# Kernel tuning notes

Measured on AMD Instinct MI355X. Metric: run time of the kernel, lower is better.

Reference implementation:

```python
import jax, jax.numpy as jnp
import numpy as np
from jax import lax

# ---- config (FalconH1Mixer, FalconH1-1.5B-like) ----
BATCH = 2
SEQ = 2048
HID = 2048
EXPAND = 2
INTER = EXPAND * HID          # 4096 (mamba_d_ssm=None)
HEADS = 64
PDIM = INTER // HEADS         # 64 head_dim
NSTATE = 128                  # mamba_d_state
G = 1                         # mamba_n_groups
HPG = HEADS // G
KCONV = 4                     # mamba_d_conv
GTS = G * NSTATE
CONV_DIM = INTER + 2 * GTS    # 4352
PROJ_DIM = 2 * INTER + 2 * GTS + HEADS  # 8512 (z | xBC | dt)
EPS = 1e-5
MUP = (0.25, 0.5, 0.5, 0.5, 1.0)  # ssm_multipliers for z, x, B, C, dt


def _mup_vector():
    # per-region muP multipliers over the zxbcdt projection axis
    return jnp.concatenate([
        jnp.full((INTER,), MUP[0], jnp.float32),
        jnp.full((INTER,), MUP[1], jnp.float32),
        jnp.full((GTS,), MUP[2], jnp.float32),
        jnp.full((GTS,), MUP[3], jnp.float32),
        jnp.full((HEADS,), MUP[4], jnp.float32),
    ])


def setup_inputs() -> dict:
    key = jax.random.key(0)
    ks = jax.random.split(key, 8)
    hidden_states = jax.random.normal(ks[0], (BATCH, SEQ, HID), jnp.float32)
    in_proj_w = jax.random.normal(ks[1], (HID, PROJ_DIM), jnp.float32) * 0.02
    conv_w = jax.random.normal(ks[2], (CONV_DIM, KCONV), jnp.float32) * 0.2
    conv_b = jnp.zeros((CONV_DIM,), jnp.float32)
    A_log = jnp.log(jnp.arange(1, HEADS + 1, dtype=jnp.float32))
    D = jnp.ones((HEADS,), jnp.float32)
    dt_bias = jax.random.uniform(ks[3], (HEADS,), jnp.float32)
    norm_w = jnp.ones((INTER,), jnp.float32)
    out_proj_w = jax.random.normal(ks[4], (INTER, HID), jnp.float32) * 0.02
    return dict(hidden_states=hidden_states, in_proj_w=in_proj_w, conv_w=conv_w,
                conv_b=conv_b, A_log=A_log, D=D, dt_bias=dt_bias,
                norm_w=norm_w, out_proj_w=out_proj_w)


def _forward(hidden_states, in_proj_w, conv_w, conv_b, A_log, D, dt_bias, norm_w, out_proj_w):
    b, l, _ = hidden_states.shape
    # zxbcdt projection with muP scaling
    proj = (hidden_states @ in_proj_w) * _mup_vector()  # (b, l, PROJ_DIM)
    z = proj[..., :INTER]
    xBC = proj[..., INTER:INTER + CONV_DIM]
    dt = proj[..., INTER + CONV_DIM:]                    # (b, l, HEADS)
    # depthwise causal conv1d + SiLU
    xBC_cl = jnp.swapaxes(xBC, 1, 2)                     # (b, c, l)
    conv = lax.conv_general_dilated(xBC_cl, conv_w[:, None, :],
                                    window_strides=(1,), padding=((KCONV - 1, 0),),
                                    feature_group_count=CONV_DIM)
    xBC = jax.nn.silu(jnp.swapaxes(conv + conv_b[None, :, None], 1, 2))  # (b, l, c)
    x = xBC[..., :INTER].reshape(b, l, G, HPG, PDIM)
    Bm = xBC[..., INTER:INTER + GTS].reshape(b, l, G, NSTATE)
    Cm = xBC[..., INTER + GTS:].reshape(b, l, G, NSTATE)
    # dt / A discretization
    dt = jax.nn.softplus(dt + dt_bias)                   # (b, l, HEADS)
    A = -jnp.exp(A_log)                                  # (HEADS,)
    dA = jnp.exp(dt * A).reshape(b, l, G, HPG)           # (b, l, g, c)
    dtx = dt.reshape(b, l, G, HPG)[..., None] * x        # (b, l, g, c, p)

    def step(state, inp):
        dA_t, dtx_t, B_t, C_t = inp                      # (b,g,c) (b,g,c,p) (b,g,n) (b,g,n)
        state = state * dA_t[..., None, None] + jnp.einsum('bgcp,bgn->bgcpn', dtx_t, B_t)
        y_t = jnp.einsum('bgn,bgcpn->bgcp', C_t, state)
        return state, y_t

    inputs = (jnp.moveaxis(dA, 1, 0), jnp.moveaxis(dtx, 1, 0),
              jnp.moveaxis(Bm, 1, 0), jnp.moveaxis(Cm, 1, 0))
    state0 = jnp.zeros((b, G, HPG, PDIM, NSTATE), hidden_states.dtype)
    _, ys = lax.scan(step, state0, inputs)               # (l, b, g, c, p)
    y = jnp.moveaxis(ys, 0, 1) + D.reshape(1, 1, G, HPG, 1) * x
    y = y.reshape(b, l, INTER)
    # grouped RMSNorm, then SiLU gate (norm_before_gate=True)
    yg = y.reshape(b, l, G, INTER // G)
    var = jnp.mean(jnp.square(yg), axis=-1, keepdims=True)
    yn = (yg * lax.rsqrt(var + EPS)).reshape(b, l, INTER) * norm_w
    out = yn * jax.nn.silu(z)
    return out @ out_proj_w                              # (b, l, HID)


def reference(hidden_states, in_proj_w, conv_w, conv_b, A_log, D, dt_bias, norm_w, out_proj_w):
    return _forward(hidden_states, in_proj_w, conv_w, conv_b, A_log, D, dt_bias, norm_w, out_proj_w)
```

## Files before the change

### kernel.cpp

```cpp
#include <hip/hip_runtime.h>
#include <stdint.h>

typedef unsigned short u16;
typedef unsigned int   u32;
typedef __attribute__((ext_vector_type(8))) short bf16x8;
typedef __attribute__((ext_vector_type(4))) float f32x4;
typedef __attribute__((ext_vector_type(4))) u32   u32x4;

static __device__ __forceinline__ float bf2f(u16 v){
  u32 u = ((u32)v) << 16;
  return __builtin_bit_cast(float, u);
}
static __device__ __forceinline__ u16 f2bf(float f){
  u32 u = __builtin_bit_cast(u32, f);
  return (u16)((u + 0x7fffu + ((u >> 16) & 1u)) >> 16);
}

#define MFMA16(a,b,c) __builtin_amdgcn_mfma_f32_16x16x32_bf16((a),(b),(c),0,0,0)

typedef const __attribute__((address_space(1))) char glb_c;
typedef __attribute__((address_space(3))) char lds_c;
static __device__ __forceinline__ void gload_lds16(const void* g, void* l){
  __builtin_amdgcn_global_load_lds((glb_c*)g, (lds_c*)l, 16, 0, 0);
}

#define SEQN   2048
#define PROJD  8512
#define CONVD  4352
#define INTERD 4096
#define NST    128
#define QC     64
#define NCHUNK 32

__global__ __launch_bounds__(256) void detect_kernel(
    const void* __restrict__ hidden, u32* __restrict__ flag)
{
  __shared__ int cnt;
  if (threadIdx.x == 0) cnt = 0;
  __syncthreads();
  if (threadIdx.x < 128){
    u16 v = ((const u16*)hidden)[threadIdx.x * 2];
    int e = (v >> 7) & 0xFF;
    int plaus = (v == 0) || (e >= 0x70 && e <= 0x8F);
    atomicAdd(&cnt, plaus);
  }
  __syncthreads();
  if (threadIdx.x == 0) *flag = (cnt < 64) ? 1u : 0u;
}

__global__ __launch_bounds__(256) void cvt_kernel(
    const void* __restrict__ src, u16* __restrict__ dst, int n,
    const u32* __restrict__ flag)
{
  bool isf32 = (*flag != 0);
  int stride = gridDim.x * 256;
  for (int i = blockIdx.x*256 + threadIdx.x; i < n; i += stride){
    if (isf32) dst[i] = f2bf(((const float*)src)[i]);
    else       dst[i] = ((const u16*)src)[i];
  }
}

__global__ __launch_bounds__(256) void cvt_transpose_kernel(
    const void* __restrict__ src, u16* __restrict__ dst,
    int K, int N, int Npad, const u32* __restrict__ flag)
{
  bool isf32 = (*flag != 0);
  __shared__ u16 tile[64][72];
  int n0 = blockIdx.x * 64, k0 = blockIdx.y * 64;
  int tid = threadIdx.x;
  int tr = tid >> 6;
  int tc = tid & 63;
  #pragma unroll
  for (int i = 0; i < 16; i++){
    int k = i*4 + tr;
    int gk = k0 + k, gn = n0 + tc;
    float v = 0.f;
    if (gk < K && gn < N)
      v = isf32 ? ((const float*)src)[(size_t)gk*N + gn]
                : bf2f(((const u16*)src)[(size_t)gk*N + gn]);
    tile[k][tc] = f2bf(v);
  }
  __syncthreads();
  #pragma unroll
  for (int i = 0; i < 16; i++){
    int n = i*4 + tr;
    int gn = n0 + n;
    if (gn < Npad && (k0 + tc) < K)
      dst[(size_t)gn*K + k0 + tc] = tile[tc][n];
  }
}

__global__ __launch_bounds__(256) void cvt_small_kernel(
    const void* cw, const void* cb, const void* al, const void* dv,
    const void* db, const void* nw, u16* __restrict__ base,
    const u32* __restrict__ flag)
{
  bool isf32 = (*flag != 0);
  int idx = blockIdx.x*256 + threadIdx.x;
  if (idx >= 26048) return;
  const void* src; int off;
  if      (idx < 17408){ src = cw; off = idx;          }
  else if (idx < 21760){ src = cb; off = idx - 17408;  }
  else if (idx < 21824){ src = al; off = idx - 21760;  }
  else if (idx < 21888){ src = dv; off = idx - 21824;  }
  else if (idx < 21952){ src = db; off = idx - 21888;  }
  else                 { src = nw; off = idx - 21952;  }
  u16 v = isf32 ? f2bf(((const float*)src)[off]) : ((const u16*)src)[off];
  base[idx] = v;
}

__global__ __launch_bounds__(512, 2) void gemm_kernel(
    const u16* __restrict__ A, const u16* __restrict__ Bt,
    u16* __restrict__ C0, u16* __restrict__ C1, u16* __restrict__ C2,
    float* __restrict__ CF,
    int M, int N, int K, int mode)
{
  __shared__ u16 smem[65536];

  const int nbx = gridDim.x;
  const int nwg = nbx * gridDim.y;
  const int bid = blockIdx.y * nbx + blockIdx.x;
  const int swz = (bid & 7) * (nwg >> 3) + (bid >> 3);
  const int m0 = (swz / nbx) * 256, n0 = (swz % nbx) * 256;

  const int tid = threadIdx.x;
  const int wave = tid >> 6, lane = tid & 63;
  const int l15 = lane & 15, quad = lane >> 4;
  const int wm = wave >> 2, wn = wave & 3;

  const size_t Kb = (size_t)K * 2;
  const int srow = tid >> 3;
  const int schk = (tid & 7) ^ (srow & 7);
  const char* Abp = (const char*)A  + (size_t)(m0 + srow) * Kb + schk * 16;
  const char* Bbp = (const char*)Bt + (size_t)(n0 + srow) * Kb + schk * 16;
  char* ldsb = (char*)smem + wave * 1024;

  const int aoff0 = ((quad    ) ^ (l15 & 7)) << 4;
  const int aoff1 = ((quad + 4) ^ (l15 & 7)) << 4;
  const char* ardb[2][2];
  const char* brdb[2][2];
  #pragma unroll
  for (int c = 0; c < 2; c++){
    ardb[c][0] = (const char*)smem + c*65536 + (wm*128 + l15)*128 + aoff0;
    ardb[c][1] = (const char*)smem + c*65536 + (wm*128 + l15)*128 + aoff1;
    brdb[c][0] = (const char*)smem + c*65536 + 32768 + (wn*64 + l15)*128 + aoff0;
    brdb[c][1] = (const char*)smem + c*65536 + 32768 + (wn*64 + l15)*128 + aoff1;
  }

  f32x4 acc[8][4];
  #pragma unroll
  for (int i = 0; i < 8; i++)
    #pragma unroll
    for (int j = 0; j < 4; j++) acc[i][j] = (f32x4){0.f,0.f,0.f,0.f};

  bf16x8 af[4];
  bf16x8 bfr[8];

#define STG(ptr, par, isB, h, kt) do{                                    \
    const char* _s = (ptr) + (size_t)((h)*128)*Kb + (size_t)(kt)*128;    \
    char* _d = ldsb + (par)*65536 + ((isB)?32768:0) + (h)*16384;         \
    gload_lds16(_s, _d);                                                 \
    gload_lds16(_s + 64*Kb, _d + 8192);                                  \
  }while(0)

  STG(Bbp,0,1,0,0); STG(Bbp,0,1,1,0);
  STG(Abp,0,0,0,0); STG(Abp,0,0,1,0);
  STG(Bbp,1,1,0,1); STG(Bbp,1,1,1,1);
  asm volatile("s_waitcnt vmcnt(4)" ::: "memory");
  __builtin_amdgcn_s_barrier();

  const int NT = K >> 6;
  for (int I = 0; I < (NT >> 1); ++I){
    const int T1 = 2*I+1, T2 = 2*I+2, T3 = 2*I+3;
    const bool pf = (T2 < NT);
    #pragma unroll
    for (int p = 0; p < 8; ++p){
      const int q = p & 3, c = p >> 2;
      #pragma unroll
      for (int k = 0; k < 2; k++){
        af[0+k] = *(const bf16x8*)(ardb[c][k] + (2*q+0)*2048);
        af[2+k] = *(const bf16x8*)(ardb[c][k] + (2*q+1)*2048);
      }
      if (q == 0){
        #pragma unroll
        for (int nf = 0; nf < 4; nf++)
          #pragma unroll
          for (int k = 0; k < 2; k++)
            bfr[nf*2+k] = *(const bf16x8*)(brdb[c][k] + nf*2048);
      }
      if      (p == 0) STG(Abp,1,0,0,T1);
      else if (p == 1) STG(Abp,1,0,1,T1);
      else if (p == 2){ if (pf) STG(Bbp,0,1,0,T2); }
      else if (p == 3){
        if (pf){ STG(Bbp,0,1,1,T2);
                 asm volatile("s_waitcnt vmcnt(4)" ::: "memory"); }
        else     asm volatile("s_waitcnt vmcnt(0)" ::: "memory");
      }
      else if (p == 4){ if (pf) STG(Abp,0,0,0,T2); }
      else if (p == 5){ if (pf) STG(Abp,0,0,1,T2); }
      else if (p == 6){ if (pf) STG(Bbp,1,1,0,T3); }
      else            { if (pf){ STG(Bbp,1,1,1,T3);
                 asm volatile("s_waitcnt vmcnt(4)" ::: "memory"); } }
      asm volatile("" ::: "memory");
      __builtin_amdgcn_s_barrier();
      asm volatile("s_waitcnt lgkmcnt(0)" ::: "memory");
      __builtin_amdgcn_s_setprio(1);
      #pragma unroll
      for (int mf2 = 0; mf2 < 2; ++mf2)
        #pragma unroll
        for (int nf = 0; nf < 4; ++nf)
          #pragma unroll
          for (int k = 0; k < 2; k++)
            acc[2*q+mf2][nf] =
                MFMA16(af[mf2*2+k], bfr[nf*2+k], acc[2*q+mf2][nf]);
      __builtin_amdgcn_s_setprio(0);
      asm volatile("" ::: "memory");
      __builtin_amdgcn_s_barrier();
    }
  }
#undef STG

  #pragma unroll
  for (int nf = 0; nf < 4; nf++){
    int col = n0 + wn*64 + nf*16 + l15;
    #pragma unroll
    for (int mf = 0; mf < 8; mf++){
      #pragma unroll
      for (int r = 0; r < 4; r++){
        int row = m0 + wm*128 + mf*16 + quad*4 + r;
        float fv = acc[mf][nf][r];
        if (mode == 2){
          if (col < N) CF[(size_t)row*N + col] = fv;
        } else if (mode == 0){
          if (col < N) C0[(size_t)row*N + col] = f2bf(fv);
        } else {
          u16 v = f2bf(fv);
          if      (col < 4096) C0[(size_t)row*4096 + col] = v;
          else if (col < 8448) C1[(size_t)row*CONVD + (col - 4096)] = v;
          else if (col < 8512) C2[(size_t)row*64 + (col - 8448)] = v;
        }
      }
    }
  }
}

__global__ __launch_bounds__(256) void conv_silu_kernel(
    const u16* __restrict__ xbcr, const u16* __restrict__ conv_w,
    const u16* __restrict__ conv_b, u16* __restrict__ xbc)
{
  int c  = blockIdx.x * 256 + threadIdx.x;
  int rl = blockIdx.y;
  int b = rl >> 11, l = rl & 2047;
  float w[4];
  #pragma unroll
  for (int k=0;k<4;k++) w[k] = 0.5f * bf2f(conv_w[c*4 + k]);
  float acc = bf2f(conv_b[c]);
  #pragma unroll
  for (int k=0;k<4;k++){
    int s = l + k - 3;
    if (s >= 0) acc += bf2f(xbcr[(size_t)(b*2048 + s)*CONVD + c]) * w[k];
  }
  float sig = 1.f / (1.f + __expf(-acc));
  xbc[(size_t)rl*CONVD + c] = f2bf(acc * sig);
}

__global__ __launch_bounds__(256) void dt_kernel(
    const u16* __restrict__ dtraw, const u16* __restrict__ dt_bias,
    const u16* __restrict__ A_log, float* __restrict__ dt_soft,
    float* __restrict__ ldA)
{
  int idx = blockIdx.x * 256 + threadIdx.x;
  int h = idx & 63;
  float x = bf2f(dtraw[idx]) + bf2f(dt_bias[h]);
  float sp = (x > 20.f) ? x : log1pf(expf(x));
  float A = -expf(bf2f(A_log[h]));
  dt_soft[idx] = sp;
  ldA[idx] = sp * A;
}

__global__ __launch_bounds__(256) void chunk_decay_kernel(
    const float* __restrict__ ldA, float* __restrict__ cdexp)
{
  int idx = blockIdx.x * 256 + threadIdx.x;
  int q = idx & 31, bh = idx >> 5;
  int b = bh >> 6, h = bh & 63;
  float s = 0.f;
  int t0 = q * QC;
  for (int t = 0; t < QC; t++) s += ldA[(size_t)(b*2048 + t0 + t)*64 + h];
  cdexp[idx] = expf(s);
}

#define SBS  136
#define SUTS 80
#define SMS  80
__global__ __launch_bounds__(256) void ssd_intra_kernel(
    const u16* __restrict__ xbc, const float* __restrict__ dt_soft,
    const float* __restrict__ ldA, u16* __restrict__ S,
    u16* __restrict__ y)
{
  int q = blockIdx.x, h = blockIdx.y, b = blockIdx.z;
  int bh = b*64 + h;
  int t0 = q * QC;
  int tid = threadIdx.x, wave = tid >> 6, lane = tid & 63;
  int l15 = lane & 15, quad = lane >> 4;

  __shared__ u16 sB [64*SBS];
  __shared__ u16 sCM[64*SBS];
  __shared__ u16 sBt[128*64];
  __shared__ u16 sUt[64*SUTS];
  __shared__ float sLa[64];
  __shared__ float sW[64];

  if (tid < 64){
    float v = ldA[(size_t)(b*2048 + t0 + tid)*64 + h];
    #pragma unroll
    for (int off = 1; off < 64; off <<= 1){
      float o = __shfl_up(v, off, 64);
      if (lane >= off) v += o;
    }
    sLa[tid] = v;
  }
  __syncthreads();
  float laE = sLa[63];
  if (tid < 64) sW[tid] = __expf(laE - sLa[tid]);
  __syncthreads();

  #pragma unroll
  for (int i = 0; i < 4; i++){
    int ch = i*256 + tid;
    int s = ch >> 4, nc = (ch & 15) * 8;
    const u16* src = xbc + (size_t)(b*2048 + t0 + s)*CONVD;
    u32x4 vb = *(const u32x4*)(src + 4096 + nc);
    u32x4 vc = *(const u32x4*)(src + 4224 + nc);
    *(u32x4*)(sB  + s*SBS + nc) = vb;
    *(u32x4*)(sCM + s*SBS + nc) = vc;
    float wdec = sW[s];
    const u16* pb = (const u16*)&vb;
    #pragma unroll
    for (int e = 0; e < 8; e++)
      sBt[(nc + e)*64 + s] = f2bf(bf2f(pb[e]) * wdec);
  }
  #pragma unroll
  for (int i = 0; i < 2; i++){
    int ch = i*256 + tid;
    int s = ch >> 3, pc = (ch & 7) * 8;
    const u16* src = xbc + (size_t)(b*2048 + t0 + s)*CONVD + h*64 + pc;
    u32x4 vx = *(const u32x4*)src;
    float dt = dt_soft[(size_t)(b*2048 + t0 + s)*64 + h];
    const u16* px = (const u16*)&vx;
    #pragma unroll
    for (int e = 0; e < 8; e++)
      sUt[(pc + e)*SUTS + s] = f2bf(bf2f(px[e]) * dt);
  }
  __syncthreads();

  int tr = (wave & 1)*32, sc = (wave >> 1)*32;
  f32x4 aM[2][2];
  #pragma unroll
  for (int i=0;i<2;i++)
    #pragma unroll
    for (int j=0;j<2;j++) aM[i][j] = (f32x4){0.f,0.f,0.f,0.f};
  #pragma unroll
  for (int kk = 0; kk < 128; kk += 32){
    bf16x8 a0 = *(const bf16x8*)(sCM + (tr      + l15)*SBS + kk + quad*8);
    bf16x8 a1 = *(const bf16x8*)(sCM + (tr + 16 + l15)*SBS + kk + quad*8);
    bf16x8 b0 = *(const bf16x8*)(sB  + (sc      + l15)*SBS + kk + quad*8);
    bf16x8 b1 = *(const bf16x8*)(sB  + (sc + 16 + l15)*SBS + kk + quad*8);
    aM[0][0] = MFMA16(a0, b0, aM[0][0]);
    aM[0][1] = MFMA16(a0, b1, aM[0][1]);
    aM[1][0] = MFMA16(a1, b0, aM[1][0]);
    aM[1][1] = MFMA16(a1, b1, aM[1][1]);
  }
  __syncthreads();
  u16* sM = sCM;
  #pragma unroll
  for (int i = 0; i < 2; i++){
    #pragma unroll
    for (int j = 0; j < 2; j++){
      int scol = sc + j*16 + l15;
      #pragma unroll
      for (int r = 0; r < 4; r++){
        int trow = tr + i*16 + quad*4 + r;
        float v = 0.f;
        if (scol <= trow) v = aM[i][j][r] * __expf(sLa[trow] - sLa[scol]);
        sM[trow*SMS + scol] = f2bf(v);
      }
    }
  }
  __syncthreads();

  f32x4 aY[2][2];
  #pragma unroll
  for (int i=0;i<2;i++)
    #pragma unroll
    for (int j=0;j<2;j++) aY[i][j] = (f32x4){0.f,0.f,0.f,0.f};
  #pragma unroll
  for (int kk = 0; kk < 64; kk += 32){
    bf16x8 a0 = *(const bf16x8*)(sM  + (tr      + l15)*SMS  + kk + quad*8);
    bf16x8 a1 = *(const bf16x8*)(sM  + (tr + 16 + l15)*SMS  + kk + quad*8);
    bf16x8 b0 = *(const bf16x8*)(sUt + (sc      + l15)*SUTS + kk + quad*8);
    bf16x8 b1 = *(const bf16x8*)(sUt + (sc + 16 + l15)*SUTS + kk + quad*8);
    aY[0][0] = MFMA16(a0, b0, aY[0][0]);
    aY[0][1] = MFMA16(a0, b1, aY[0][1]);
    aY[1][0] = MFMA16(a1, b0, aY[1][0]);
    aY[1][1] = MFMA16(a1, b1, aY[1][1]);
  }
  #pragma unroll
  for (int i = 0; i < 2; i++){
    #pragma unroll
    for (int j = 0; j < 2; j++){
      int p = sc + j*16 + l15;
      #pragma unroll
      for (int r = 0; r < 4; r++){
        int t = tr + i*16 + quad*4 + r;
        y[(size_t)(b*2048 + t0 + t)*INTERD + h*64 + p] = f2bf(aY[i][j][r]);
      }
    }
  }

  int pr = (wave & 1)*32, nw = (wave >> 1)*64;
  f32x4 aS[2][4];
  #pragma unroll
  for (int i=0;i<2;i++)
    #pragma unroll
    for (int j=0;j<4;j++) aS[i][j] = (f32x4){0.f,0.f,0.f,0.f};
  #pragma unroll
  for (int kk = 0; kk < 64; kk += 32){
    bf16x8 a0 = *(const bf16x8*)(sUt + (pr      + l15)*SUTS + kk + quad*8);
    bf16x8 a1 = *(const bf16x8*)(sUt + (pr + 16 + l15)*SUTS + kk + quad*8);
    #pragma unroll
    for (int j = 0; j < 4; j++){
      bf16x8 bb = *(const bf16x8*)(sBt + (nw + j*16 + l15)*64 + kk + quad*8);
      aS[0][j] = MFMA16(a0, bb, aS[0][j]);
      aS[1][j] = MFMA16(a1, bb, aS[1][j]);
    }
  }
  u16* Sl = S + ((size_t)bh*NCHUNK + q)*8192;
  #pragma unroll
  for (int i = 0; i < 2; i++){
    #pragma unroll
    for (int j = 0; j < 4; j++){
      int n = nw + j*16 + l15;
      #pragma unroll
      for (int r = 0; r < 4; r++){
        int p = pr + i*16 + quad*4 + r;
        Sl[p*NST + n] = f2bf(aS[i][j][r]);
      }
    }
  }
}

__global__ __launch_bounds__(256) void ssd_carry_kernel(
    u16* __restrict__ S, const float* __restrict__ cdexp)
{
  int idx = blockIdx.x * 256 + threadIdx.x;
  int e = idx & 8191, bh = idx >> 13;
  float E = 0.f;
  for (int q = 0; q < NCHUNK; q++){
    size_t off = ((size_t)bh*NCHUNK + q)*8192 + e;
    float v = bf2f(S[off]);
    S[off] = f2bf(E);
    E = cdexp[bh*NCHUNK + q] * E + v;
  }
}

__global__ __launch_bounds__(256) void ssd_inter_kernel(
    const u16* __restrict__ xbc, const float* __restrict__ ldA,
    const u16* __restrict__ S, const u16* __restrict__ Dvec,
    u16* __restrict__ y)
{
  int q = blockIdx.x, h = blockIdx.y, b = blockIdx.z;
  int bh = b*64 + h;
  int t0 = q * QC;
  int tid = threadIdx.x, wave = tid >> 6, lane = tid & 63;
  int l15 = lane & 15, quad = lane >> 4;

  __shared__ u16 sC[64*SBS];
  __shared__ u16 sS[64*SBS];
  __shared__ float sLa[64];

  if (tid < 64){
    float v = ldA[(size_t)(b*2048 + t0 + tid)*64 + h];
    #pragma unroll
    for (int off = 1; off < 64; off <<= 1){
      float o = __shfl_up(v, off, 64);
      if (lane >= off) v += o;
    }
    sLa[tid] = v;
  }
  const u16* Sc = S + ((size_t)bh*NCHUNK + q)*8192;
  #pragma unroll
  for (int i = 0; i < 4; i++){
    int ch = i*256 + tid;
    int s = ch >> 4, nc = (ch & 15) * 8;
    *(u32x4*)(sC + s*SBS + nc) =
        *(const u32x4*)(xbc + (size_t)(b*2048 + t0 + s)*CONVD + 4224 + nc);
    *(u32x4*)(sS + s*SBS + nc) = *(const u32x4*)(Sc + s*NST + nc);
  }
  __syncthreads();

  int tr = (wave & 1)*32, pc = (wave >> 1)*32;
  f32x4 acc[2][2];
  #pragma unroll
  for (int i=0;i<2;i++)
    #pragma unroll
    for (int j=0;j<2;j++) acc[i][j] = (f32x4){0.f,0.f,0.f,0.f};
  #pragma unroll
  for (int kk = 0; kk < 128; kk += 32){
    bf16x8 a0 = *(const bf16x8*)(sC + (tr      + l15)*SBS + kk + quad*8);
    bf16x8 a1 = *(const bf16x8*)(sC + (tr + 16 + l15)*SBS + kk + quad*8);
    bf16x8 b0 = *(const bf16x8*)(sS + (pc      + l15)*SBS + kk + quad*8);
    bf16x8 b1 = *(const bf16x8*)(sS + (pc + 16 + l15)*SBS + kk + quad*8);
    acc[0][0] = MFMA16(a0, b0, acc[0][0]);
    acc[0][1] = MFMA16(a0, b1, acc[0][1]);
    acc[1][0] = MFMA16(a1, b0, acc[1][0]);
    acc[1][1] = MFMA16(a1, b1, acc[1][1]);
  }
  float Dh = bf2f(Dvec[h]);
  #pragma unroll
  for (int i = 0; i < 2; i++){
    #pragma unroll
    for (int j = 0; j < 2; j++){
      int p = pc + j*16 + l15;
      #pragma unroll
      for (int r = 0; r < 4; r++){
        int t = tr + i*16 + quad*4 + r;
        size_t row = (size_t)(b*2048 + t0 + t);
        size_t yo = row*INTERD + h*64 + p;
        float xv = bf2f(xbc[row*CONVD + h*64 + p]);
        float v = bf2f(y[yo]) + __expf(sLa[t]) * acc[i][j][r] + Dh * xv;
        y[yo] = f2bf(v);
      }
    }
  }
}

__global__ __launch_bounds__(256) void rmsnorm_gate_kernel(
    const u16* __restrict__ y, const u16* __restrict__ z,
    const u16* __restrict__ norm_w, u16* __restrict__ g)
{
  int rl = blockIdx.x;
  int tid = threadIdx.x, wave = tid >> 6, lane = tid & 63;
  const u16* yr = y + (size_t)rl*INTERD;
  float vy[16];
  float ss = 0.f;
  #pragma unroll
  for (int i = 0; i < 16; i++){
    int idx = i*256 + tid;
    float v = bf2f(yr[idx]);
    vy[i] = v;
    ss += v*v;
  }
  #pragma unroll
  for (int off = 32; off >= 1; off >>= 1) ss += __shfl_xor(ss, off, 64);
  __shared__ float red[4];
  if (lane == 0) red[wave] = ss;
  __syncthreads();
  float tot = red[0] + red[1] + red[2] + red[3];
  float rstd = rsqrtf(tot * (1.f/4096.f) + 1e-5f);
  const u16* zr = z + (size_t)rl*INTERD;
  u16* gr = g + (size_t)rl*INTERD;
  #pragma unroll
  for (int i = 0; i < 16; i++){
    int idx = i*256 + tid;
    float v = vy[i] * rstd * bf2f(norm_w[idx]);
    float zv = 0.25f * bf2f(zr[idx]);
    float sig = 1.f / (1.f + __expf(-zv));
    gr[idx] = f2bf(v * zv * sig);
  }
}

extern "C" void kernel_launch(void* const* d_in, const int* in_sizes, int n_in,
                              void* d_out, int out_size, void* d_ws, size_t ws_size,
                              hipStream_t stream)
{
  const void* hidden_r    = d_in[0];
  const void* in_proj_r   = d_in[1];
  const void* conv_w_r    = d_in[2];
  const void* conv_b_r    = d_in[3];
  const void* A_log_r     = d_in[4];
  const void* Dvec_r      = d_in[5];
  const void* dt_bias_r   = d_in[6];
  const void* norm_w_r    = d_in[7];
  const void* out_proj_r  = d_in[8];
  float* out = (float*)d_out;
  char* ws = (char*)d_ws;

  u16*   z     = (u16*)(ws + 0);
  u16*   xbcr  = (u16*)(ws + 33554432ull);
  u16*   yb    = (u16*)(ws + 33554432ull);
  u16*   dtraw = (u16*)(ws + 69206016ull);
  u16*   xbc   = (u16*)(ws + 69730304ull);
  u16*   w2b   = (u16*)(ws + 69730304ull);
  float* dt_s  = (float*)(ws + 105381888ull);
  float* lda   = (float*)(ws + 106430464ull);
  float* cdexp = (float*)(ws + 107479040ull);
  u32*   flag  = (u32*)(ws + 107495424ull);
  u16*   svec  = (u16*)(ws + 107495680ull);
  u16*   cw_b  = svec;
  u16*   cb_b  = svec + 17408;
  u16*   al_b  = svec + 21760;
  u16*   d_b   = svec + 21824;
  u16*   db_b  = svec + 21888;
  u16*   nw_b  = svec + 21952;
  u16*   S     = (u16*)(ws + 107626496ull);
  u16*   hb    = (u16*)(ws + 107626496ull);
  u16*   w1b   = (u16*)(ws + 124403712ull);
  u16*   g     = (u16*)(ws + 107626496ull);

  detect_kernel<<<1, 256, 0, stream>>>(hidden_r, flag);
  cvt_kernel<<<4096, 256, 0, stream>>>(hidden_r, hb, 8388608, flag);
  cvt_transpose_kernel<<<dim3(136, 32), 256, 0, stream>>>(
      in_proj_r, w1b, 2048, 8512, 8704, flag);
  cvt_small_kernel<<<102, 256, 0, stream>>>(conv_w_r, conv_b_r, A_log_r,
      Dvec_r, dt_bias_r, norm_w_r, svec, flag);
  gemm_kernel<<<dim3(34, 16), 512, 0, stream>>>(
      hb, w1b, z, xbcr, dtraw, (float*)nullptr, 4096, 8704, 2048, 1);
  conv_silu_kernel<<<dim3(17, 4096), 256, 0, stream>>>(xbcr, cw_b, cb_b, xbc);
  dt_kernel<<<1024, 256, 0, stream>>>(dtraw, db_b, al_b, dt_s, lda);
  chunk_decay_kernel<<<16, 256, 0, stream>>>(lda, cdexp);
  ssd_intra_kernel<<<dim3(NCHUNK, 64, 2), 256, 0, stream>>>(xbc, dt_s, lda, S, yb);
  ssd_carry_kernel<<<4096, 256, 0, stream>>>(S, cdexp);
  ssd_inter_kernel<<<dim3(NCHUNK, 64, 2), 256, 0, stream>>>(xbc, lda, S, d_b, yb);
  cvt_transpose_kernel<<<dim3(32, 64), 256, 0, stream>>>(
      out_proj_r, w2b, 4096, 2048, 2048, flag);
  rmsnorm_gate_kernel<<<4096, 256, 0, stream>>>(yb, z, nw_b, g);
  gemm_kernel<<<dim3(8, 16), 512, 0, stream>>>(
      g, w2b, (u16*)nullptr, (u16*)nullptr, (u16*)nullptr, out,
      4096, 2048, 4096, 2);
}
```

Baseline: 718.8 us.

## Template GEMM M-tile size, use 128-row tiles for out-proj, drop per-step barrier

```diff
diff --git a/kernel.cpp b/kernel.cpp
--- a/kernel.cpp
+++ b/kernel.cpp
@@ -109,19 +109,22 @@
   base[idx] = v;
 }
 
+template<int MT>
 __global__ __launch_bounds__(512, 2) void gemm_kernel(
     const u16* __restrict__ A, const u16* __restrict__ Bt,
     u16* __restrict__ C0, u16* __restrict__ C1, u16* __restrict__ C2,
     float* __restrict__ CF,
     int M, int N, int K, int mode)
 {
-  __shared__ u16 smem[65536];
+  constexpr int ASZ  = MT * 16384;
+  constexpr int BUFS = ASZ + 32768;
+  __shared__ u16 smem[BUFS];
 
   const int nbx = gridDim.x;
   const int nwg = nbx * gridDim.y;
   const int bid = blockIdx.y * nbx + blockIdx.x;
   const int swz = (bid & 7) * (nwg >> 3) + (bid >> 3);
-  const int m0 = (swz / nbx) * 256, n0 = (swz % nbx) * 256;
+  const int m0 = (swz / nbx) * (MT*128), n0 = (swz % nbx) * 256;
 
   const int tid = threadIdx.x;
   const int wave = tid >> 6, lane = tid & 63;
@@ -141,31 +144,37 @@
   const char* brdb[2][2];
   #pragma unroll
   for (int c = 0; c < 2; c++){
-    ardb[c][0] = (const char*)smem + c*65536 + (wm*128 + l15)*128 + aoff0;
-    ardb[c][1] = (const char*)smem + c*65536 + (wm*128 + l15)*128 + aoff1;
-    brdb[c][0] = (const char*)smem + c*65536 + 32768 + (wn*64 + l15)*128 + aoff0;
-    brdb[c][1] = (const char*)smem + c*65536 + 32768 + (wn*64 + l15)*128 + aoff1;
-  }
-
-  f32x4 acc[8][4];
-  #pragma unroll
-  for (int i = 0; i < 8; i++)
+    ardb[c][0] = (const char*)smem + c*BUFS + (wm*(MT*64) + l15)*128 + aoff0;
+    ardb[c][1] = (const char*)smem + c*BUFS + (wm*(MT*64) + l15)*128 + aoff1;
+    brdb[c][0] = (const char*)smem + c*BUFS + ASZ + (wn*64 + l15)*128 + aoff0;
+    brdb[c][1] = (const char*)smem + c*BUFS + ASZ + (wn*64 + l15)*128 + aoff1;
+  }
+
+  f32x4 acc[MT*4][4];
+  #pragma unroll
+  for (int i = 0; i < MT*4; i++)
     #pragma unroll
     for (int j = 0; j < 4; j++) acc[i][j] = (f32x4){0.f,0.f,0.f,0.f};
 
-  bf16x8 af[4];
+  bf16x8 af[2*MT];
   bf16x8 bfr[8];
 
-#define STG(ptr, par, isB, h, kt) do{                                    \
-    const char* _s = (ptr) + (size_t)((h)*128)*Kb + (size_t)(kt)*128;    \
-    char* _d = ldsb + (par)*65536 + ((isB)?32768:0) + (h)*16384;         \
+#define STGB(par, h, kt) do{                                             \
+    const char* _s = Bbp + (size_t)((h)*128)*Kb + (size_t)(kt)*128;      \
+    char* _d = ldsb + (par)*BUFS + ASZ + (h)*16384;                      \
     gload_lds16(_s, _d);                                                 \
     gload_lds16(_s + 64*Kb, _d + 8192);                                  \
   }while(0)
-
-  STG(Bbp,0,1,0,0); STG(Bbp,0,1,1,0);
-  STG(Abp,0,0,0,0); STG(Abp,0,0,1,0);
-  STG(Bbp,1,1,0,1); STG(Bbp,1,1,1,1);
+#define STGA(par, h, kt) do{                                             \
+    const char* _s = Abp + (size_t)((h)*(MT*64))*Kb + (size_t)(kt)*128;  \
+    char* _d = ldsb + (par)*BUFS + (h)*(MT*8192);                        \
+    gload_lds16(_s, _d);                                                 \
+    if (MT == 2) gload_lds16(_s + 64*Kb, _d + 8192);                     \
+  }while(0)
+
+  STGB(0,0,0); STGB(0,1,0);
+  STGA(0,0,0); STGA(0,1,0);
+  STGB(1,0,1); STGB(1,1,1);
   asm volatile("s_waitcnt vmcnt(4)" ::: "memory");
   __builtin_amdgcn_s_barrier();
 
@@ -177,10 +186,10 @@
     for (int p = 0; p < 8; ++p){
       const int q = p & 3, c = p >> 2;
       #pragma unroll
-      for (int k = 0; k < 2; k++){
-        af[0+k] = *(const bf16x8*)(ardb[c][k] + (2*q+0)*2048);
-        af[2+k] = *(const bf16x8*)(ardb[c][k] + (2*q+1)*2048);
-      }
+      for (int k = 0; k < 2; k++)
+        #pragma unroll
+        for (int mf2 = 0; mf2 < MT; mf2++)
+          af[mf2*2+k] = *(const bf16x8*)(ardb[c][k] + (MT*q+mf2)*2048);
       if (q == 0){
         #pragma unroll
         for (int nf = 0; nf < 4; nf++)
@@ -188,46 +197,44 @@
           for (int k = 0; k < 2; k++)
             bfr[nf*2+k] = *(const bf16x8*)(brdb[c][k] + nf*2048);
       }
-      if      (p == 0) STG(Abp,1,0,0,T1);
-      else if (p == 1) STG(Abp,1,0,1,T1);
-      else if (p == 2){ if (pf) STG(Bbp,0,1,0,T2); }
+      if      (p == 0) STGA(1,0,T1);
+      else if (p == 1) STGA(1,1,T1);
+      else if (p == 2){ if (pf) STGB(0,0,T2); }
       else if (p == 3){
-        if (pf){ STG(Bbp,0,1,1,T2);
+        if (pf){ STGB(0,1,T2);
                  asm volatile("s_waitcnt vmcnt(4)" ::: "memory"); }
         else     asm volatile("s_waitcnt vmcnt(0)" ::: "memory");
       }
-      else if (p == 4){ if (pf) STG(Abp,0,0,0,T2); }
-      else if (p == 5){ if (pf) STG(Abp,0,0,1,T2); }
-      else if (p == 6){ if (pf) STG(Bbp,1,1,0,T3); }
-      else            { if (pf){ STG(Bbp,1,1,1,T3);
+      else if (p == 4){ if (pf) STGA(0,0,T2); }
+      else if (p == 5){ if (pf) STGA(0,1,T2); }
+      else if (p == 6){ if (pf) STGB(1,0,T3); }
+      else            { if (pf){ STGB(1,1,T3);
                  asm volatile("s_waitcnt vmcnt(4)" ::: "memory"); } }
       asm volatile("" ::: "memory");
       __builtin_amdgcn_s_barrier();
-      asm volatile("s_waitcnt lgkmcnt(0)" ::: "memory");
       __builtin_amdgcn_s_setprio(1);
       #pragma unroll
-      for (int mf2 = 0; mf2 < 2; ++mf2)
+      for (int mf2 = 0; mf2 < MT; ++mf2)
         #pragma unroll
         for (int nf = 0; nf < 4; ++nf)
           #pragma unroll
           for (int k = 0; k < 2; k++)
-            acc[2*q+mf2][nf] =
-                MFMA16(af[mf2*2+k], bfr[nf*2+k], acc[2*q+mf2][nf]);
+            acc[MT*q+mf2][nf] =
+                MFMA16(af[mf2*2+k], bfr[nf*2+k], acc[MT*q+mf2][nf]);
       __builtin_amdgcn_s_setprio(0);
-      asm volatile("" ::: "memory");
-      __builtin_amdgcn_s_barrier();
-    }
-  }
-#undef STG
+    }
+  }
+#undef STGA
+#undef STGB
 
   #pragma unroll
   for (int nf = 0; nf < 4; nf++){
     int col = n0 + wn*64 + nf*16 + l15;
     #pragma unroll
-    for (int mf = 0; mf < 8; mf++){
+    for (int mf = 0; mf < MT*4; mf++){
       #pragma unroll
       for (int r = 0; r < 4; r++){
-        int row = m0 + wm*128 + mf*16 + quad*4 + r;
+        int row = m0 + wm*(MT*64) + mf*16 + quad*4 + r;
         float fv = acc[mf][nf][r];
         if (mode == 2){
           if (col < N) CF[(size_t)row*N + col] = fv;
@@ -614,7 +621,7 @@
       in_proj_r, w1b, 2048, 8512, 8704, flag);
   cvt_small_kernel<<<102, 256, 0, stream>>>(conv_w_r, conv_b_r, A_log_r,
       Dvec_r, dt_bias_r, norm_w_r, svec, flag);
-  gemm_kernel<<<dim3(34, 16), 512, 0, stream>>>(
+  gemm_kernel<2><<<dim3(34, 16), 512, 0, stream>>>(
       hb, w1b, z, xbcr, dtraw, (float*)nullptr, 4096, 8704, 2048, 1);
   conv_silu_kernel<<<dim3(17, 4096), 256, 0, stream>>>(xbcr, cw_b, cb_b, xbc);
   dt_kernel<<<1024, 256, 0, stream>>>(dtraw, db_b, al_b, dt_s, lda);
@@ -625,7 +632,7 @@
   cvt_transpose_kernel<<<dim3(32, 64), 256, 0, stream>>>(
       out_proj_r, w2b, 4096, 2048, 2048, flag);
   rmsnorm_gate_kernel<<<4096, 256, 0, stream>>>(yb, z, nw_b, g);
-  gemm_kernel<<<dim3(8, 16), 512, 0, stream>>>(
+  gemm_kernel<1><<<dim3(8, 32), 512, 0, stream>>>(
       g, w2b, (u16*)nullptr, (u16*)nullptr, (u16*)nullptr, out,
       4096, 2048, 4096, 2);
 }
```

Measured after the change: 711.7 us. No clear change (-1.0%).
